# Performance work log

Hardware: AMD Instinct MI355X
Metric: run time of the kernel (lower is better)

Reference implementation:

```python
import jax, jax.numpy as jnp
import numpy as np

B, N, D_IN = 4, 2048, 1024
H, D_OUT = 8, 128


def setup_inputs() -> dict:
    key = jax.random.key(0)
    k1, k2, k3 = jax.random.split(key, 3)
    x = jax.random.normal(k1, (B, N, D_IN), dtype=jnp.float32)
    # W: (num_head, 3 [q,k,v], d_in, output_dim), glorot-ish scale
    W = jax.random.normal(k2, (H, 3, D_IN, D_OUT), dtype=jnp.float32) * (1.0 / np.sqrt(D_IN))
    Wo = jax.random.normal(k3, (H * D_OUT, D_OUT), dtype=jnp.float32) * (1.0 / np.sqrt(H * D_OUT))
    return {"x": x, "W": W, "Wo": Wo}


def reference(x, W, Wo):
    # Per-head QKV projections, vectorized over heads.
    # q,k,v: [B, H, N, D_OUT]
    q = jnp.einsum("bnd,hde->bhne", x, W[:, 0])
    k = jnp.einsum("bnd,hde->bhne", x, W[:, 1])
    v = jnp.einsum("bnd,hde->bhne", x, W[:, 2])
    scale = 1.0 / jnp.sqrt(jnp.asarray(D_OUT, dtype=x.dtype))
    # scores: [B, H, N, N]
    e = jnp.einsum("bhne,bhme->bhnm", q, k) * scale
    a = jax.nn.softmax(e, axis=-1)
    o = jnp.einsum("bhnm,bhme->bhne", a, v)  # [B, H, N, D_OUT]
    # concat heads -> [B, N, H*D_OUT]; head i occupies slice [i*D_OUT:(i+1)*D_OUT]
    o = jnp.transpose(o, (0, 2, 1, 3)).reshape(x.shape[0], x.shape[1], H * D_OUT)
    z = jnp.einsum("bnf,fe->bne", o, Wo)  # [B, N, D_OUT]
    return z
```

## Files before the change

### kernel.cpp

```cpp
#include <hip/hip_runtime.h>
#include <cstdint>


#define DEV __device__ __forceinline__

typedef _Float16 h8 __attribute__((ext_vector_type(8)));
typedef _Float16 h4 __attribute__((ext_vector_type(4)));
typedef _Float16 h2 __attribute__((ext_vector_type(2)));
typedef float f4 __attribute__((ext_vector_type(4)));
typedef float f16x16 __attribute__((ext_vector_type(16)));
typedef uint32_t u32x4 __attribute__((ext_vector_type(4)));
typedef uint32_t u32x2 __attribute__((ext_vector_type(2)));

typedef __attribute__((address_space(1))) const uint32_t gu32;
typedef __attribute__((address_space(3))) uint32_t lu32;

DEV float fexp2(float x) { return __builtin_amdgcn_exp2f(x); }

DEV f4 mfma16(h8 a, h8 b, f4 c) {
  return __builtin_amdgcn_mfma_f32_16x16x32_f16(a, b, c, 0, 0, 0);
}

DEV f16x16 mfma32(h8 a, h8 b, f16x16 c) {
  return __builtin_amdgcn_mfma_f32_32x32x16_f16(a, b, c, 0, 0, 0);
}

DEV void g2l16(void* lds, const void* g) {
  __builtin_amdgcn_global_load_lds((gu32*)(uintptr_t)g, (lu32*)(uintptr_t)lds,
                                   16, 0, 0);
}

DEV uint32_t pkrn(float a, float b) {
  h2 t;
  t[0] = (_Float16)a;
  t[1] = (_Float16)b;
  return __builtin_bit_cast(uint32_t, t);
}

DEV u32x2 pl32swap(uint32_t x, uint32_t y) {
  return __builtin_amdgcn_permlane32_swap(x, y, false, false);
}

__global__ __launch_bounds__(256) void cvt_all_kernel(
    const float* __restrict__ x, _Float16* __restrict__ Xb,
    const float* __restrict__ W, const float* __restrict__ Wo,
    _Float16* __restrict__ WT, _Float16* __restrict__ WoT) {
  __shared__ float st[64][68];
  const int bid = blockIdx.x;
  const int tid = threadIdx.x;
  if (bid < 8192) {
    size_t i = (size_t)(bid * 256 + tid) * 4;
    f4 v = *(const f4*)(x + i);
    h4 o;
    o[0] = (_Float16)v[0];
    o[1] = (_Float16)v[1];
    o[2] = (_Float16)v[2];
    o[3] = (_Float16)v[3];
    *(h4*)(Xb + i) = o;
    return;
  }
  const int idx0 = bid - 8192;
  const int mz = idx0 >> 5;
  const int rem = idx0 & 31;
  const int d0 = (rem & 15) * 64;
  const int e0 = (rem >> 4) * 64;
  const float* src = (mz < 24) ? (W + (size_t)mz * 131072) : Wo;
  _Float16* dst = (mz < 24) ? (WT + (size_t)mz * 131072) : WoT;
#pragma unroll
  for (int r = 0; r < 4; ++r) {
    int idx = r * 256 + tid;
    int dd = idx >> 4, cc = (idx & 15) * 4;
    f4 v = *(const f4*)(src + (size_t)(d0 + dd) * 128 + e0 + cc);
    *(f4*)&st[dd][cc] = v;
  }
  __syncthreads();
#pragma unroll
  for (int r = 0; r < 2; ++r) {
    int idx = r * 256 + tid;
    int ee = idx >> 3, dd = (idx & 7) * 8;
    h8 o;
#pragma unroll
    for (int i = 0; i < 8; ++i) o[i] = (_Float16)st[dd + i][ee];
    *(h8*)(dst + (size_t)(e0 + ee) * 1024 + d0 + dd) = o;
  }
}

__global__ __launch_bounds__(256, 2) void gemm_qkv_kernel(
    const _Float16* __restrict__ A, const _Float16* __restrict__ BTall,
    _Float16* __restrict__ Qb, _Float16* __restrict__ Kb,
    _Float16* __restrict__ VTb) {
  __shared__ __align__(16) _Float16 sAB[2][16384];
  const int tid = threadIdx.x;
  const int wave = tid >> 6, lane = tid & 63;
  const int g = lane >> 4, l15 = lane & 15;
  const int sw = l15 & 7;
  const int m0 = blockIdx.x * 128;
  const int j = blockIdx.y;
  const _Float16* BT = BTall + (size_t)j * (128 * 1024);

  f4 acc[4][4] = {};
  const int ar = (wave >> 1) * 64 + l15;
  const int br = (wave & 1) * 64 + l15;

#define QSTAGE(buf, kt)                                                        \
  {                                                                            \
    _Float16* dA = &sAB[buf][0];                                               \
    _Float16* dB = &sAB[buf][8192];                                            \
    _Pragma("unroll") for (int i = 0; i < 4; ++i) {                            \
      int idx = i * 256 + tid;                                                 \
      int row = idx >> 3;                                                      \
      int jg = (idx & 7) ^ (row & 7);   \
      g2l16(dA + idx * 8, A + (size_t)(m0 + row) * 1024 + (kt) + jg * 8);      \
      g2l16(dB + idx * 8, BT + (size_t)row * 1024 + (kt) + jg * 8);            \
    }                                                                          \
  }

  QSTAGE(0, 0);
  int cur = 0;
#pragma unroll 1
  for (int t = 0; t < 16; ++t) {
    __syncthreads();
    if (t < 15) QSTAGE(cur ^ 1, (t + 1) * 64);
    const _Float16* bA = &sAB[cur][0];
    const _Float16* bB = &sAB[cur][8192];
#pragma unroll
    for (int ks = 0; ks < 2; ++ks) {
      int off = ((ks * 4 + g) ^ sw) * 8;
      h8 af[4], bf[4];
#pragma unroll
      for (int mt = 0; mt < 4; ++mt)
        af[mt] = *(const h8*)&bA[(ar + mt * 16) * 64 + off];
#pragma unroll
      for (int nt = 0; nt < 4; ++nt)
        bf[nt] = *(const h8*)&bB[(br + nt * 16) * 64 + off];
#pragma unroll
      for (int mt = 0; mt < 4; ++mt)
#pragma unroll
        for (int nt = 0; nt < 4; ++nt)
          acc[mt][nt] = mfma16(af[mt], bf[nt], acc[mt][nt]);
    }
    cur ^= 1;
  }
#undef QSTAGE

  _Float16* sE = &sAB[0][0];
  const int wr = (wave >> 1) * 64, wc = (wave & 1) * 64;
  const int h = j / 3, s = j - h * 3;
  if (s < 2) {
    const float scl = (s == 0) ? 0.12751741032075984f : 1.0f;
    _Float16* dst = (s == 0) ? Qb : Kb;
    __syncthreads();
#pragma unroll
    for (int mt = 0; mt < 4; ++mt)
#pragma unroll
      for (int rg = 0; rg < 4; ++rg) {
        int rl = wr + mt * 16 + g * 4 + rg;
#pragma unroll
        for (int nt = 0; nt < 4; ++nt) {
          int c = wc + nt * 16 + l15;
          sE[rl * 128 + (((c >> 3) ^ (rl & 7)) * 8) + (c & 7)] =
              (_Float16)(acc[mt][nt][rg] * scl);
        }
      }
    __syncthreads();
    int rr = tid >> 1, seg = tid & 1;
    int m = m0 + rr, b = m >> 11, n = m & 2047;
    size_t rb = ((size_t)((b * 8 + h) * 2048 + n)) * 128;
#pragma unroll
    for (int k = 0; k < 8; ++k) {
      int ch = seg * 8 + k;
      h8 v = *(const h8*)&sE[rr * 128 + ((ch ^ (rr & 7)) * 8)];
      *(h8*)&dst[rb + ch * 8] = v;
    }
  } else {
    __syncthreads();
    const int b = m0 >> 11, n0 = m0 & 2047;
    size_t base = (size_t)(b * 8 + h) * (128 * 2048);
#pragma unroll
    for (int mt = 0; mt < 4; ++mt)
#pragma unroll
      for (int rg = 0; rg < 4; ++rg) {
        int nl = wr + mt * 16 + g * 4 + rg;
        int cc = (nl >> 3), ci = nl & 7;
#pragma unroll
        for (int nt = 0; nt < 4; ++nt) {
          int c = wc + nt * 16 + l15;
          sE[c * 128 + ((cc ^ (c & 7)) * 8) + ci] = (_Float16)acc[mt][nt][rg];
        }
      }
    __syncthreads();
    int c = tid >> 1, seg = tid & 1;
#pragma unroll
    for (int k = 0; k < 8; ++k) {
      int ch = seg * 8 + k;
      h8 v = *(const h8*)&sE[c * 128 + ((ch ^ (c & 7)) * 8)];
      *(h8*)&VTb[base + (size_t)c * 2048 + n0 + ch * 8] = v;
    }
  }
}

__global__ __launch_bounds__(256, 2) void flash_kernel(
    const _Float16* __restrict__ Qb, const _Float16* __restrict__ Kb,
    const _Float16* __restrict__ VTb, _Float16* __restrict__ Oc) {
  __shared__ __align__(16) _Float16 sK[2][64 * 128];
  __shared__ __align__(16) _Float16 sVT[2][128 * 64];
  const int tid = threadIdx.x, wave = tid >> 6, lane = tid & 63;
  const int l31 = lane & 31, hi = lane >> 5;
  const int sw = l31 & 7;
  const int bh = blockIdx.x, b = bh >> 3, h = bh & 7;
  const int q0 = blockIdx.y * 128;
  const _Float16* Q = Qb + (size_t)bh * (2048 * 128);
  const _Float16* Kp = Kb + (size_t)bh * (2048 * 128);
  const _Float16* VT = VTb + (size_t)bh * (128 * 2048);

  h8 qf[8];
#pragma unroll
  for (int c = 0; c < 8; ++c)
    qf[c] = *(const h8*)&Q[(size_t)(q0 + wave * 32 + l31) * 128 + c * 16 +
                           hi * 8];

  f16x16 oacc[4] = {};
  float lsum = 0.0f;

#define STAGE(buf, kv0)                                                        \
  {                                                                            \
    _Float16* dK = &sK[buf][0];                                                \
    _Float16* dV = &sVT[buf][0];                                               \
    _Pragma("unroll") for (int i = 0; i < 4; ++i) {                            \
      int idx = i * 256 + tid;                                                 \
      int rk = idx >> 4, ck = idx & 15;                                        \
      g2l16(dK + idx * 8,                                                      \
            Kp + (size_t)((kv0) + rk) * 128 + ((ck ^ (rk & 7)) * 8));          \
      int rv = idx >> 3, cv = idx & 7;                                         \
      g2l16(dV + idx * 8,                                                      \
            VT + (size_t)rv * 2048 + (kv0) + ((cv ^ (rv & 7)) * 8));           \
    }                                                                          \
  }

  STAGE(0, 0);
  int cur = 0;
#pragma unroll 1
  for (int t = 0; t < 32; ++t) {
    __syncthreads();
    if (t < 31) STAGE(cur ^ 1, (t + 1) * 64);
    const _Float16* bK = &sK[cur][0];
    const _Float16* bV = &sVT[cur][0];

    f16x16 s0 = {}, s1 = {};
#pragma unroll
    for (int c = 0; c < 8; ++c) {
      int off = ((c * 2 + hi) ^ sw) * 8;
      h8 a0 = *(const h8*)&bK[l31 * 128 + off];
      h8 a1 = *(const h8*)&bK[(32 + l31) * 128 + off];
      s0 = mfma32(a0, qf[c], s0);
      s1 = mfma32(a1, qf[c], s1);
    }

    uint32_t w0[8], w1[8];
#pragma unroll
    for (int j = 0; j < 8; ++j) {
      float a0 = fexp2(s0[2 * j]), b0 = fexp2(s0[2 * j + 1]);
      float a1 = fexp2(s1[2 * j]), b1 = fexp2(s1[2 * j + 1]);
      lsum += (a0 + b0) + (a1 + b1);
      w0[j] = pkrn(a0, b0);
      w1[j] = pkrn(a1, b1);
    }

    h8 pf[4];
#pragma unroll
    for (int half = 0; half < 2; ++half) {
      u32x2 r0 = pl32swap(w0[half * 4 + 0], w0[half * 4 + 2]);
      u32x2 r1 = pl32swap(w0[half * 4 + 1], w0[half * 4 + 3]);
      u32x4 tt;
      tt[0] = r0[0];
      tt[1] = r1[0];
      tt[2] = r0[1];
      tt[3] = r1[1];
      pf[half] = __builtin_bit_cast(h8, tt);
      u32x2 r2 = pl32swap(w1[half * 4 + 0], w1[half * 4 + 2]);
      u32x2 r3 = pl32swap(w1[half * 4 + 1], w1[half * 4 + 3]);
      u32x4 uu;
      uu[0] = r2[0];
      uu[1] = r3[0];
      uu[2] = r2[1];
      uu[3] = r3[1];
      pf[2 + half] = __builtin_bit_cast(h8, uu);
    }

#pragma unroll
    for (int dt = 0; dt < 4; ++dt) {
#pragma unroll
      for (int c = 0; c < 4; ++c) {
        int off = ((c * 2 + hi) ^ sw) * 8;
        h8 vf = *(const h8*)&bV[(dt * 32 + l31) * 64 + off];
        oacc[dt] = mfma32(vf, pf[c], oacc[dt]);
      }
    }
    cur ^= 1;
  }
#undef STAGE

  lsum += __shfl_xor(lsum, 32, 64);
  const float inv = 1.0f / lsum;

  __syncthreads();
  _Float16* sO = &sK[0][0] + wave * 4096;
#pragma unroll
  for (int dt = 0; dt < 4; ++dt)
#pragma unroll
    for (int r = 0; r < 16; ++r) {
      int d = dt * 32 + (r & 3) + 8 * (r >> 2) + 4 * hi;
      sO[l31 * 128 + (d ^ (sw << 3))] = (_Float16)(oacc[dt][r] * inv);
    }
  const int l15 = lane & 15, gq = lane >> 4;
#pragma unroll
  for (int it = 0; it < 8; ++it) {
    int q = it * 4 + gq;
    h8 v = *(const h8*)&sO[q * 128 + ((l15 ^ (q & 7)) * 8)];
    int n = q0 + wave * 32 + q;
    *(h8*)&Oc[((size_t)(b * 2048 + n)) * 1024 + h * 128 + l15 * 8] = v;
  }
}

__global__ __launch_bounds__(256, 2) void gemm_out_kernel(
    const _Float16* __restrict__ A, const _Float16* __restrict__ BT,
    float* __restrict__ outF) {
  __shared__ __align__(16) _Float16 sA[2][16 * 128];
  __shared__ __align__(16) _Float16 sB[2][128 * 128];
  const int tid = threadIdx.x, wave = tid >> 6, lane = tid & 63;
  const int g = lane >> 4, l15 = lane & 15, sw = l15 & 7;
  const int m0 = blockIdx.x * 16;
  f4 acc[2] = {};

#define OSTAGE(buf, kt)                                                        \
  {                                                                            \
    int rowa = tid >> 4, cka = tid & 15;                                       \
    int jga = cka ^ (rowa & 7);                                                \
    g2l16(&sA[buf][tid * 8], A + (size_t)(m0 + rowa) * 1024 + (kt) + jga * 8); \
    _Pragma("unroll") for (int i = 0; i < 8; ++i) {                            \
      int idx = i * 256 + tid;                                                 \
      int row = idx >> 4, ck = idx & 15;                                       \
      int jg = ck ^ (row & 7);                                                 \
      g2l16(&sB[buf][idx * 8], BT + (size_t)row * 1024 + (kt) + jg * 8);       \
    }                                                                          \
  }

  OSTAGE(0, 0);
  int cur = 0;
#pragma unroll 1
  for (int t = 0; t < 8; ++t) {
    __syncthreads();
    if (t < 7) OSTAGE(cur ^ 1, (t + 1) * 128);
#pragma unroll
    for (int ks = 0; ks < 4; ++ks) {
      int off = ((ks * 4 + g) ^ sw) * 8;
      h8 af = *(const h8*)&sA[cur][l15 * 128 + off];
#pragma unroll
      for (int nt = 0; nt < 2; ++nt) {
        h8 bf = *(const h8*)&sB[cur][(wave * 32 + nt * 16 + l15) * 128 + off];
        acc[nt] = mfma16(af, bf, acc[nt]);
      }
    }
    cur ^= 1;
  }
#undef OSTAGE
#pragma unroll
  for (int rg = 0; rg < 4; ++rg) {
    int m = m0 + g * 4 + rg;
#pragma unroll
    for (int nt = 0; nt < 2; ++nt)
      outF[(size_t)m * 128 + wave * 32 + nt * 16 + l15] = acc[nt][rg];
  }
}

extern "C" void kernel_launch(void* const* d_in, const int* in_sizes, int n_in,
                              void* d_out, int out_size, void* d_ws,
                              size_t ws_size, hipStream_t stream) {
  const float* x = (const float*)d_in[0];
  const float* W = (const float*)d_in[1];
  const float* Wo = (const float*)d_in[2];
  float* out = (float*)d_out;
  char* ws = (char*)d_ws;

  _Float16* Xb = (_Float16*)(ws + 0);
  _Float16* WT = (_Float16*)(ws + 16777216);
  _Float16* WoT = (_Float16*)(ws + 23068672);
  _Float16* Qb = (_Float16*)(ws + 23330816);
  _Float16* Kb = (_Float16*)(ws + 40108032);
  _Float16* VTb = (_Float16*)(ws + 56885248);
  _Float16* Oc = (_Float16*)(ws + 73662464);

  cvt_all_kernel<<<8992, 256, 0, stream>>>(x, Xb, W, Wo, WT, WoT);
  gemm_qkv_kernel<<<dim3(64, 24), 256, 0, stream>>>(Xb, WT, Qb, Kb, VTb);
  flash_kernel<<<dim3(32, 16), 256, 0, stream>>>(Qb, Kb, VTb, Oc);
  gemm_out_kernel<<<512, 256, 0, stream>>>(Oc, WoT, out);
}
```

Before: 228.3 us.

## Load V fragments directly from global into registers, widen K swizzle

The flash kernel no longer stages V^T tiles through shared memory. Each wave loads its V fragments straight from global memory into 16 h8 registers at the top of every KV iteration, and only K is double-buffered in LDS. The K swizzle is widened from 8 to 16 chunks to reduce bank conflicts. This halves LDS usage, which may allow higher occupancy, but adds global-load latency inside the loop and raises register pressure, and every wave re-reads V from global or L2.

```diff
diff --git a/kernel.cpp b/kernel.cpp
--- a/kernel.cpp
+++ b/kernel.cpp
@@ -203,10 +203,9 @@
     const _Float16* __restrict__ Qb, const _Float16* __restrict__ Kb,
     const _Float16* __restrict__ VTb, _Float16* __restrict__ Oc) {
   __shared__ __align__(16) _Float16 sK[2][64 * 128];
-  __shared__ __align__(16) _Float16 sVT[2][128 * 64];
   const int tid = threadIdx.x, wave = tid >> 6, lane = tid & 63;
   const int l31 = lane & 31, hi = lane >> 5;
-  const int sw = l31 & 7;
+  const int sw4 = l31 & 15;
   const int bh = blockIdx.x, b = bh >> 3, h = bh & 7;
   const int q0 = blockIdx.y * 128;
   const _Float16* Q = Qb + (size_t)bh * (2048 * 128);
@@ -225,15 +224,11 @@
 #define STAGE(buf, kv0)                                                        \
   {                                                                            \
     _Float16* dK = &sK[buf][0];                                                \
-    _Float16* dV = &sVT[buf][0];                                               \
     _Pragma("unroll") for (int i = 0; i < 4; ++i) {                            \
       int idx = i * 256 + tid;                                                 \
       int rk = idx >> 4, ck = idx & 15;                                        \
       g2l16(dK + idx * 8,                                                      \
-            Kp + (size_t)((kv0) + rk) * 128 + ((ck ^ (rk & 7)) * 8));          \
-      int rv = idx >> 3, cv = idx & 7;                                         \
-      g2l16(dV + idx * 8,                                                      \
-            VT + (size_t)rv * 2048 + (kv0) + ((cv ^ (rv & 7)) * 8));           \
+            Kp + (size_t)((kv0) + rk) * 128 + ((ck ^ (rk & 15)) * 8));         \
     }                                                                          \
   }
 
@@ -242,14 +237,21 @@
 #pragma unroll 1
   for (int t = 0; t < 32; ++t) {
     __syncthreads();
-    if (t < 31) STAGE(cur ^ 1, (t + 1) * 64);
+    const int kv0 = t * 64;
+    h8 vf[16];
+#pragma unroll
+    for (int dt = 0; dt < 4; ++dt)
+#pragma unroll
+      for (int c = 0; c < 4; ++c)
+        vf[dt * 4 + c] = *(const h8*)&VT[(size_t)(dt * 32 + l31) * 2048 + kv0 +
+                                         c * 16 + hi * 8];
+    if (t < 31) STAGE(cur ^ 1, kv0 + 64);
     const _Float16* bK = &sK[cur][0];
-    const _Float16* bV = &sVT[cur][0];
 
     f16x16 s0 = {}, s1 = {};
 #pragma unroll
     for (int c = 0; c < 8; ++c) {
-      int off = ((c * 2 + hi) ^ sw) * 8;
+      int off = ((c * 2 + hi) ^ sw4) * 8;
       h8 a0 = *(const h8*)&bK[l31 * 128 + off];
       h8 a1 = *(const h8*)&bK[(32 + l31) * 128 + off];
       s0 = mfma32(a0, qf[c], s0);
@@ -288,14 +290,10 @@
     }
 
 #pragma unroll
-    for (int dt = 0; dt < 4; ++dt) {
-#pragma unroll
-      for (int c = 0; c < 4; ++c) {
-        int off = ((c * 2 + hi) ^ sw) * 8;
-        h8 vf = *(const h8*)&bV[(dt * 32 + l31) * 64 + off];
-        oacc[dt] = mfma32(vf, pf[c], oacc[dt]);
-      }
-    }
+    for (int dt = 0; dt < 4; ++dt)
+#pragma unroll
+      for (int c = 0; c < 4; ++c)
+        oacc[dt] = mfma32(vf[dt * 4 + c], pf[c], oacc[dt]);
     cur ^= 1;
   }
 #undef STAGE
@@ -310,7 +308,7 @@
 #pragma unroll
     for (int r = 0; r < 16; ++r) {
       int d = dt * 32 + (r & 3) + 8 * (r >> 2) + 4 * hi;
-      sO[l31 * 128 + (d ^ (sw << 3))] = (_Float16)(oacc[dt][r] * inv);
+      sO[l31 * 128 + (d ^ ((l31 & 7) << 3))] = (_Float16)(oacc[dt][r] * inv);
     }
   const int l15 = lane & 15, gq = lane >> 4;
 #pragma unroll
```

Result: slower. 307.6 us (+34.7%).
